# Optimization experiments

Measured on AMD Instinct MI355X. Metric: run time of the kernel, lower is better.

Reference implementation:

```python
import jax, jax.numpy as jnp
import numpy as np

B, C, H, W = 32, 3072, 28, 28
L1 = 9            # num_landmarks + 1 (background)
NUM_CLASSES = 200


def setup_inputs() -> dict:
    key = jax.random.key(0)
    k1, k2, k3 = jax.random.split(key, 3)
    feat = jax.random.normal(k1, (B, C, H, W), dtype=jnp.float32)
    w_land = jax.random.normal(k2, (L1, C), dtype=jnp.float32) * 0.02  # fc_landmarks 1x1 conv weight
    modulation = jnp.ones((1, C, L1), dtype=jnp.float32)
    w_cls = jax.random.normal(k3, (NUM_CLASSES, C), dtype=jnp.float32) * 0.02
    return {"feat": feat, "w_land": w_land, "modulation": modulation, "w_cls": w_cls}


def reference(feat, w_land, modulation, w_cls):
    # fc_landmarks: 1x1 conv == per-pixel GEMM. ab: (B, L1, H, W)
    ab = jnp.einsum('bchw,lc->blhw', feat, w_land)
    # squared distance to each landmark 'code': ||x||^2 - 2<x,w> + ||w||^2
    b_sq = jnp.sum(feat * feat, axis=1, keepdims=True)            # (B,1,H,W)
    a_sq = jnp.sum(w_land * w_land, axis=1)[None, :, None, None]  # (1,L1,1,1)
    dist = b_sq - 2.0 * ab + a_sq                                 # (B,L1,H,W)
    maps = jax.nn.softmax(-dist, axis=1)                          # softmax over landmarks
    # (maps.unsqueeze(1) * x.unsqueeze(2)).mean(-1).mean(-1)  ->  weighted spatial pooling
    # expressed as a contraction instead of materializing (B,C,L1,H,W)
    all_features = jnp.einsum('bchw,blhw->bcl', feat, maps) / (H * W)  # (B,C,L1)
    all_features_mod = all_features * modulation                       # 'original' modulation
    # drop background landmark, linear classifier per landmark (eval: dropout = identity)
    scores = jnp.einsum('bcl,kc->bkl', all_features_mod[..., :-1], w_cls)  # (B,num_classes,L)
    # modulation_orth = False -> return all_features (pre-modulation)
    return (all_features, maps, scores, dist)
```

## Files before the change

### kernel.cpp

```cpp
#include <hip/hip_runtime.h>

#define BB 32
#define CC 3072
#define HWD 784
#define L1 9
#define NCLS 200
#define CSPLIT 8
#define CCHUNK 384

#define AF_OFF     0
#define MAPS_OFF   884736
#define SCORES_OFF 1110528
#define DIST_OFF   1161728

__global__ __launch_bounds__(256) void kA(const float* __restrict__ feat,
                                          const float* __restrict__ w_land,
                                          float* __restrict__ partial) {
    __shared__ __align__(16) float ws[L1 * CCHUNK];
    const int tid = threadIdx.x;
    const int b = blockIdx.x >> 2, pb = blockIdx.x & 3;
    const int cs = blockIdx.y;
    for (int i = tid; i < L1 * CCHUNK; i += 256) {
        int l = i / CCHUNK, cc = i - l * CCHUNK;
        ws[i] = w_land[l * CC + cs * CCHUNK + cc];
    }
    __syncthreads();
    const int pix = pb * 256 + tid;
    if (pix >= HWD) return;

    float ab[L1];
    #pragma unroll
    for (int l = 0; l < L1; ++l) ab[l] = 0.f;
    float bsq = 0.f;

    const float* fp = feat + ((size_t)b * CC + (size_t)cs * CCHUNK) * HWD + pix;
    for (int cc = 0; cc < CCHUNK; cc += 4) {
        float v0 = fp[(size_t)(cc + 0) * HWD];
        float v1 = fp[(size_t)(cc + 1) * HWD];
        float v2 = fp[(size_t)(cc + 2) * HWD];
        float v3 = fp[(size_t)(cc + 3) * HWD];
        bsq += v0 * v0 + v1 * v1 + v2 * v2 + v3 * v3;
        #pragma unroll
        for (int l = 0; l < L1; ++l) {
            const float4 w4 = *(const float4*)&ws[l * CCHUNK + cc];
            ab[l] += v0 * w4.x + v1 * w4.y + v2 * w4.z + v3 * w4.w;
        }
    }
    float* out = partial + (((size_t)b * HWD + pix) * CSPLIT + cs) * 10;
    #pragma unroll
    for (int l = 0; l < L1; ++l) out[l] = ab[l];
    out[L1] = bsq;
}

__global__ __launch_bounds__(256) void kB(const float* __restrict__ w_land,
                                          const float* __restrict__ partial,
                                          float* __restrict__ maps_out,
                                          float* __restrict__ dist_out) {
    __shared__ float asq_s[4][L1];
    const int tid = threadIdx.x;
    const int lane = tid & 63, wv = tid >> 6;

    float s[L1];
    #pragma unroll
    for (int l = 0; l < L1; ++l) s[l] = 0.f;
    for (int c = tid; c < CC; c += 256) {
        #pragma unroll
        for (int l = 0; l < L1; ++l) {
            float w = w_land[l * CC + c];
            s[l] += w * w;
        }
    }
    #pragma unroll
    for (int l = 0; l < L1; ++l) {
        float v = s[l];
        for (int off = 32; off; off >>= 1) v += __shfl_xor(v, off);
        s[l] = v;
    }
    if (lane == 0) {
        #pragma unroll
        for (int l = 0; l < L1; ++l) asq_s[wv][l] = s[l];
    }
    __syncthreads();

    const int b = blockIdx.x >> 2, pb = blockIdx.x & 3;
    const int pix = pb * 256 + tid;
    if (pix >= HWD) return;

    float asq[L1];
    #pragma unroll
    for (int l = 0; l < L1; ++l)
        asq[l] = asq_s[0][l] + asq_s[1][l] + asq_s[2][l] + asq_s[3][l];

    const float* pp = partial + ((size_t)b * HWD + pix) * (CSPLIT * 10);
    float ab[L1], bsq = 0.f;
    #pragma unroll
    for (int l = 0; l < L1; ++l) ab[l] = 0.f;
    for (int cs = 0; cs < CSPLIT; ++cs) {
        #pragma unroll
        for (int l = 0; l < L1; ++l) ab[l] += pp[cs * 10 + l];
        bsq += pp[cs * 10 + L1];
    }

    float d[L1], mn = 1e30f;
    #pragma unroll
    for (int l = 0; l < L1; ++l) {
        d[l] = bsq - 2.f * ab[l] + asq[l];
        mn = fminf(mn, d[l]);
    }
    float e[L1], sum = 0.f;
    #pragma unroll
    for (int l = 0; l < L1; ++l) {
        e[l] = expf(mn - d[l]);
        sum += e[l];
    }
    const float inv = 1.f / sum;
    #pragma unroll
    for (int l = 0; l < L1; ++l) {
        size_t o = ((size_t)b * L1 + l) * HWD + pix;
        maps_out[o] = e[l] * inv;
        dist_out[o] = d[l];
    }
}

__global__ __launch_bounds__(256) void kC(const float* __restrict__ feat,
                                          const float* __restrict__ maps,
                                          const float* __restrict__ modulation,
                                          float* __restrict__ af_out,
                                          float* __restrict__ afT) {
    __shared__ __align__(16) float ms[L1 * HWD];
    const int tid = threadIdx.x;
    const int b = blockIdx.y;
    const float* mb = maps + (size_t)b * L1 * HWD;
    for (int i = tid; i < L1 * HWD; i += 256) ms[i] = mb[i];
    __syncthreads();

    const int wv = tid >> 6, lane = tid & 63;
    const int c0 = blockIdx.x * 16 + wv * 4;
    const float* fb = feat + ((size_t)b * CC + c0) * HWD;

    float acc[4][L1];
    #pragma unroll
    for (int j = 0; j < 4; ++j)
        #pragma unroll
        for (int l = 0; l < L1; ++l) acc[j][l] = 0.f;

    for (int g = lane; g < HWD / 4; g += 64) {
        const int p4 = g * 4;
        float4 m4[L1];
        #pragma unroll
        for (int l = 0; l < L1; ++l) m4[l] = *(const float4*)&ms[l * HWD + p4];
        #pragma unroll
        for (int j = 0; j < 4; ++j) {
            const float4 f = *(const float4*)&fb[(size_t)j * HWD + p4];
            #pragma unroll
            for (int l = 0; l < L1; ++l)
                acc[j][l] += f.x * m4[l].x + f.y * m4[l].y + f.z * m4[l].z + f.w * m4[l].w;
        }
    }
    #pragma unroll
    for (int j = 0; j < 4; ++j)
        #pragma unroll
        for (int l = 0; l < L1; ++l) {
            float v = acc[j][l];
            for (int off = 32; off; off >>= 1) v += __shfl_xor(v, off);
            acc[j][l] = v;
        }
    if (lane == 0) {
        #pragma unroll
        for (int j = 0; j < 4; ++j) {
            const int c = c0 + j;
            #pragma unroll
            for (int l = 0; l < L1; ++l) {
                const float v = acc[j][l] * (1.f / (float)HWD);
                af_out[((size_t)b * CC + c) * L1 + l] = v;
                if (l < 8)
                    afT[((size_t)b * 8 + l) * CC + c] = v * modulation[c * L1 + l];
            }
        }
    }
}

__global__ __launch_bounds__(256) void kD(const float* __restrict__ afT,
                                          const float* __restrict__ w_cls,
                                          float* __restrict__ scores) {
    const int wid = blockIdx.x * 4 + (threadIdx.x >> 6);
    const int lane = threadIdx.x & 63;
    const int b = wid / NCLS, k = wid - b * NCLS;
    const float* wk = w_cls + (size_t)k * CC;
    const float* at = afT + (size_t)b * 8 * CC;
    float acc[8];
    #pragma unroll
    for (int l = 0; l < 8; ++l) acc[l] = 0.f;
    for (int c = lane; c < CC; c += 64) {
        const float wv = wk[c];
        #pragma unroll
        for (int l = 0; l < 8; ++l) acc[l] += wv * at[(size_t)l * CC + c];
    }
    #pragma unroll
    for (int l = 0; l < 8; ++l) {
        float v = acc[l];
        for (int off = 32; off; off >>= 1) v += __shfl_xor(v, off);
        acc[l] = v;
    }
    if (lane == 0) {
        #pragma unroll
        for (int l = 0; l < 8; ++l)
            scores[((size_t)b * NCLS + k) * 8 + l] = acc[l];
    }
}

extern "C" void kernel_launch(void* const* d_in, const int* in_sizes, int n_in,
                              void* d_out, int out_size, void* d_ws, size_t ws_size,
                              hipStream_t stream) {
    const float* feat       = (const float*)d_in[0];
    const float* w_land     = (const float*)d_in[1];
    const float* modulation = (const float*)d_in[2];
    const float* w_cls      = (const float*)d_in[3];

    float* out    = (float*)d_out;
    float* af     = out + AF_OFF;
    float* maps   = out + MAPS_OFF;
    float* scores = out + SCORES_OFF;
    float* dist   = out + DIST_OFF;

    float* partial = (float*)d_ws;
    float* afT     = partial + (size_t)BB * HWD * 80;

    kA<<<dim3(BB * 4, CSPLIT), 256, 0, stream>>>(feat, w_land, partial);
    kB<<<BB * 4, 256, 0, stream>>>(w_land, partial, maps, dist);
    kC<<<dim3(CC / 16, BB), 256, 0, stream>>>(feat, maps, modulation, af, afT);
    kD<<<BB * NCLS / 4, 256, 0, stream>>>(afT, w_cls, scores);
}
```

Before: 585.6 us.

## Restructure landmark GEMM with float4 pixel loads, transposed weights, and wider classifier

Adds a kernel that transposes w_land into a padded per-channel layout and precomputes partial squared norms. kA now reads feat as float4 over pixels, with more channel splits and weights read through the scalar/global path. The partial buffer layout becomes planar so kB reads it coalesced. kC drops the shared-memory staging of maps in favor of direct global loads. kD computes two classes per wave with float4 loads. The net effect depends on whether the extra partial traffic and the uncached weight reads offset the gains from the wider loads.

```diff
diff --git a/kernel.cpp b/kernel.cpp
--- a/kernel.cpp
+++ b/kernel.cpp
@@ -5,100 +5,116 @@
 #define HWD 784
 #define L1 9
 #define NCLS 200
-#define CSPLIT 8
-#define CCHUNK 384
+#define CSPLIT 32
+#define CCHUNK 96
+#define WROW 12
 
 #define AF_OFF     0
 #define MAPS_OFF   884736
 #define SCORES_OFF 1110528
 #define DIST_OFF   1161728
 
-__global__ __launch_bounds__(256) void kA(const float* __restrict__ feat,
-                                          const float* __restrict__ w_land,
-                                          float* __restrict__ partial) {
-    __shared__ __align__(16) float ws[L1 * CCHUNK];
+#define P_OFF   0
+#define P_CNT   (BB*CSPLIT*10*HWD)
+#define WT_OFF  (P_OFF + P_CNT)
+#define WT_CNT  (CC*WROW)
+#define ASQ_OFF (WT_OFF + WT_CNT)
+#define ASQ_CNT (12*WROW)
+#define AFT_OFF (ASQ_OFF + ASQ_CNT)
+
+__global__ __launch_bounds__(256) void kW(const float* __restrict__ w_land,
+                                          float* __restrict__ wT,
+                                          float* __restrict__ asqp) {
+    __shared__ float red[4][L1];
     const int tid = threadIdx.x;
-    const int b = blockIdx.x >> 2, pb = blockIdx.x & 3;
-    const int cs = blockIdx.y;
-    for (int i = tid; i < L1 * CCHUNK; i += 256) {
-        int l = i / CCHUNK, cc = i - l * CCHUNK;
-        ws[i] = w_land[l * CC + cs * CCHUNK + cc];
-    }
-    __syncthreads();
-    const int pix = pb * 256 + tid;
-    if (pix >= HWD) return;
-
-    float ab[L1];
-    #pragma unroll
-    for (int l = 0; l < L1; ++l) ab[l] = 0.f;
-    float bsq = 0.f;
-
-    const float* fp = feat + ((size_t)b * CC + (size_t)cs * CCHUNK) * HWD + pix;
-    for (int cc = 0; cc < CCHUNK; cc += 4) {
-        float v0 = fp[(size_t)(cc + 0) * HWD];
-        float v1 = fp[(size_t)(cc + 1) * HWD];
-        float v2 = fp[(size_t)(cc + 2) * HWD];
-        float v3 = fp[(size_t)(cc + 3) * HWD];
-        bsq += v0 * v0 + v1 * v1 + v2 * v2 + v3 * v3;
-        #pragma unroll
-        for (int l = 0; l < L1; ++l) {
-            const float4 w4 = *(const float4*)&ws[l * CCHUNK + cc];
-            ab[l] += v0 * w4.x + v1 * w4.y + v2 * w4.z + v3 * w4.w;
-        }
-    }
-    float* out = partial + (((size_t)b * HWD + pix) * CSPLIT + cs) * 10;
-    #pragma unroll
-    for (int l = 0; l < L1; ++l) out[l] = ab[l];
-    out[L1] = bsq;
-}
-
-__global__ __launch_bounds__(256) void kB(const float* __restrict__ w_land,
-                                          const float* __restrict__ partial,
-                                          float* __restrict__ maps_out,
-                                          float* __restrict__ dist_out) {
-    __shared__ float asq_s[4][L1];
-    const int tid = threadIdx.x;
-    const int lane = tid & 63, wv = tid >> 6;
-
-    float s[L1];
-    #pragma unroll
-    for (int l = 0; l < L1; ++l) s[l] = 0.f;
-    for (int c = tid; c < CC; c += 256) {
-        #pragma unroll
-        for (int l = 0; l < L1; ++l) {
-            float w = w_land[l * CC + c];
-            s[l] += w * w;
-        }
-    }
+    const int c = blockIdx.x * 256 + tid;
+    float w[L1], s[L1];
+    #pragma unroll
+    for (int l = 0; l < L1; ++l) w[l] = w_land[l * CC + c];
+    #pragma unroll
+    for (int l = 0; l < L1; ++l) { wT[c * WROW + l] = w[l]; s[l] = w[l] * w[l]; }
+    wT[c * WROW + 9] = 0.f; wT[c * WROW + 10] = 0.f; wT[c * WROW + 11] = 0.f;
     #pragma unroll
     for (int l = 0; l < L1; ++l) {
         float v = s[l];
         for (int off = 32; off; off >>= 1) v += __shfl_xor(v, off);
         s[l] = v;
     }
+    const int lane = tid & 63, wv = tid >> 6;
     if (lane == 0) {
         #pragma unroll
-        for (int l = 0; l < L1; ++l) asq_s[wv][l] = s[l];
+        for (int l = 0; l < L1; ++l) red[wv][l] = s[l];
     }
     __syncthreads();
-
+    if (tid == 0) {
+        #pragma unroll
+        for (int l = 0; l < L1; ++l)
+            asqp[blockIdx.x * WROW + l] = red[0][l] + red[1][l] + red[2][l] + red[3][l];
+    }
+}
+
+__global__ __launch_bounds__(256) void kA(const float* __restrict__ feat,
+                                          const float* __restrict__ wT,
+                                          float* __restrict__ partial) {
+    const int tid = threadIdx.x;
+    if (tid >= HWD / 4) return;
+    const int b = blockIdx.x, cs = blockIdx.y;
+    const int p4 = tid * 4;
+    const float* fp = feat + ((size_t)b * CC + (size_t)cs * CCHUNK) * HWD + p4;
+    const float* wp = wT + (size_t)cs * CCHUNK * WROW;
+
+    float abx[L1], aby[L1], abz[L1], abw[L1];
+    #pragma unroll
+    for (int l = 0; l < L1; ++l) { abx[l] = 0.f; aby[l] = 0.f; abz[l] = 0.f; abw[l] = 0.f; }
+    float bx = 0.f, by = 0.f, bz = 0.f, bw = 0.f;
+
+    #pragma unroll 4
+    for (int c = 0; c < CCHUNK; ++c) {
+        const float4 f = *(const float4*)&fp[(size_t)c * HWD];
+        bx += f.x * f.x; by += f.y * f.y; bz += f.z * f.z; bw += f.w * f.w;
+        #pragma unroll
+        for (int l = 0; l < L1; ++l) {
+            const float w = wp[c * WROW + l];
+            abx[l] += f.x * w; aby[l] += f.y * w; abz[l] += f.z * w; abw[l] += f.w * w;
+        }
+    }
+    float* pout = partial + (size_t)(b * CSPLIT + cs) * 10 * HWD + p4;
+    #pragma unroll
+    for (int l = 0; l < L1; ++l) {
+        float4 o; o.x = abx[l]; o.y = aby[l]; o.z = abz[l]; o.w = abw[l];
+        *(float4*)&pout[(size_t)l * HWD] = o;
+    }
+    float4 o; o.x = bx; o.y = by; o.z = bz; o.w = bw;
+    *(float4*)&pout[(size_t)9 * HWD] = o;
+}
+
+__global__ __launch_bounds__(256) void kB(const float* __restrict__ partial,
+                                          const float* __restrict__ asqp,
+                                          float* __restrict__ maps_out,
+                                          float* __restrict__ dist_out) {
     const int b = blockIdx.x >> 2, pb = blockIdx.x & 3;
-    const int pix = pb * 256 + tid;
+    const int pix = pb * 256 + threadIdx.x;
     if (pix >= HWD) return;
 
     float asq[L1];
     #pragma unroll
-    for (int l = 0; l < L1; ++l)
-        asq[l] = asq_s[0][l] + asq_s[1][l] + asq_s[2][l] + asq_s[3][l];
-
-    const float* pp = partial + ((size_t)b * HWD + pix) * (CSPLIT * 10);
+    for (int l = 0; l < L1; ++l) {
+        float s = 0.f;
+        #pragma unroll
+        for (int bc = 0; bc < 12; ++bc) s += asqp[bc * WROW + l];
+        asq[l] = s;
+    }
+
     float ab[L1], bsq = 0.f;
     #pragma unroll
     for (int l = 0; l < L1; ++l) ab[l] = 0.f;
+    const float* pp = partial + (size_t)b * CSPLIT * 10 * HWD + pix;
+    #pragma unroll 4
     for (int cs = 0; cs < CSPLIT; ++cs) {
-        #pragma unroll
-        for (int l = 0; l < L1; ++l) ab[l] += pp[cs * 10 + l];
-        bsq += pp[cs * 10 + L1];
+        const float* q = pp + (size_t)cs * 10 * HWD;
+        #pragma unroll
+        for (int l = 0; l < L1; ++l) ab[l] += q[(size_t)l * HWD];
+        bsq += q[(size_t)9 * HWD];
     }
 
     float d[L1], mn = 1e30f;
@@ -110,13 +126,13 @@
     float e[L1], sum = 0.f;
     #pragma unroll
     for (int l = 0; l < L1; ++l) {
-        e[l] = expf(mn - d[l]);
+        e[l] = __expf(mn - d[l]);
         sum += e[l];
     }
     const float inv = 1.f / sum;
     #pragma unroll
     for (int l = 0; l < L1; ++l) {
-        size_t o = ((size_t)b * L1 + l) * HWD + pix;
+        const size_t o = ((size_t)b * L1 + l) * HWD + pix;
         maps_out[o] = e[l] * inv;
         dist_out[o] = d[l];
     }
@@ -127,16 +143,11 @@
                                           const float* __restrict__ modulation,
                                           float* __restrict__ af_out,
                                           float* __restrict__ afT) {
-    __shared__ __align__(16) float ms[L1 * HWD];
-    const int tid = threadIdx.x;
+    const int wv = threadIdx.x >> 6, lane = threadIdx.x & 63;
     const int b = blockIdx.y;
-    const float* mb = maps + (size_t)b * L1 * HWD;
-    for (int i = tid; i < L1 * HWD; i += 256) ms[i] = mb[i];
-    __syncthreads();
-
-    const int wv = tid >> 6, lane = tid & 63;
     const int c0 = blockIdx.x * 16 + wv * 4;
     const float* fb = feat + ((size_t)b * CC + c0) * HWD;
+    const float* mb = maps + (size_t)b * L1 * HWD;
 
     float acc[4][L1];
     #pragma unroll
@@ -148,7 +159,7 @@
         const int p4 = g * 4;
         float4 m4[L1];
         #pragma unroll
-        for (int l = 0; l < L1; ++l) m4[l] = *(const float4*)&ms[l * HWD + p4];
+        for (int l = 0; l < L1; ++l) m4[l] = *(const float4*)&mb[(size_t)l * HWD + p4];
         #pragma unroll
         for (int j = 0; j < 4; ++j) {
             const float4 f = *(const float4*)&fb[(size_t)j * HWD + p4];
@@ -185,27 +196,44 @@
                                           float* __restrict__ scores) {
     const int wid = blockIdx.x * 4 + (threadIdx.x >> 6);
     const int lane = threadIdx.x & 63;
-    const int b = wid / NCLS, k = wid - b * NCLS;
-    const float* wk = w_cls + (size_t)k * CC;
+    const int b = wid / (NCLS / 2), kp = wid - b * (NCLS / 2);
+    const int k0 = kp * 2;
     const float* at = afT + (size_t)b * 8 * CC;
-    float acc[8];
-    #pragma unroll
-    for (int l = 0; l < 8; ++l) acc[l] = 0.f;
-    for (int c = lane; c < CC; c += 64) {
-        const float wv = wk[c];
-        #pragma unroll
-        for (int l = 0; l < 8; ++l) acc[l] += wv * at[(size_t)l * CC + c];
-    }
-    #pragma unroll
-    for (int l = 0; l < 8; ++l) {
-        float v = acc[l];
-        for (int off = 32; off; off >>= 1) v += __shfl_xor(v, off);
-        acc[l] = v;
-    }
+    const float* w0 = w_cls + (size_t)k0 * CC;
+    const float* w1 = w0 + CC;
+
+    float acc[2][8];
+    #pragma unroll
+    for (int kk = 0; kk < 2; ++kk)
+        #pragma unroll
+        for (int l = 0; l < 8; ++l) acc[kk][l] = 0.f;
+
+    #pragma unroll 2
+    for (int it = 0; it < CC / 256; ++it) {
+        const int c4 = (lane + it * 64) * 4;
+        const float4 wa = *(const float4*)&w0[c4];
+        const float4 wb = *(const float4*)&w1[c4];
+        #pragma unroll
+        for (int l = 0; l < 8; ++l) {
+            const float4 a = *(const float4*)&at[(size_t)l * CC + c4];
+            acc[0][l] += wa.x * a.x + wa.y * a.y + wa.z * a.z + wa.w * a.w;
+            acc[1][l] += wb.x * a.x + wb.y * a.y + wb.z * a.z + wb.w * a.w;
+        }
+    }
+    #pragma unroll
+    for (int kk = 0; kk < 2; ++kk)
+        #pragma unroll
+        for (int l = 0; l < 8; ++l) {
+            float v = acc[kk][l];
+            for (int off = 32; off; off >>= 1) v += __shfl_xor(v, off);
+            acc[kk][l] = v;
+        }
     if (lane == 0) {
         #pragma unroll
-        for (int l = 0; l < 8; ++l)
-            scores[((size_t)b * NCLS + k) * 8 + l] = acc[l];
+        for (int kk = 0; kk < 2; ++kk)
+            #pragma unroll
+            for (int l = 0; l < 8; ++l)
+                scores[((size_t)b * NCLS + k0 + kk) * 8 + l] = acc[kk][l];
     }
 }
 
@@ -223,11 +251,15 @@
     float* scores = out + SCORES_OFF;
     float* dist   = out + DIST_OFF;
 
-    float* partial = (float*)d_ws;
-    float* afT     = partial + (size_t)BB * HWD * 80;
-
-    kA<<<dim3(BB * 4, CSPLIT), 256, 0, stream>>>(feat, w_land, partial);
-    kB<<<BB * 4, 256, 0, stream>>>(w_land, partial, maps, dist);
+    float* ws      = (float*)d_ws;
+    float* partial = ws + P_OFF;
+    float* wT      = ws + WT_OFF;
+    float* asqp    = ws + ASQ_OFF;
+    float* afT     = ws + AFT_OFF;
+
+    kW<<<CC / 256, 256, 0, stream>>>(w_land, wT, asqp);
+    kA<<<dim3(BB, CSPLIT), 256, 0, stream>>>(feat, wT, partial);
+    kB<<<BB * 4, 256, 0, stream>>>(partial, asqp, maps, dist);
     kC<<<dim3(CC / 16, BB), 256, 0, stream>>>(feat, maps, modulation, af, afT);
-    kD<<<BB * NCLS / 4, 256, 0, stream>>>(afT, w_cls, scores);
-}
+    kD<<<BB * NCLS / 2 / 4, 256, 0, stream>>>(afT, w_cls, scores);
+}
```

After: 519.5 us. 11.3% less time.
